# Kernel optimization log

Measured on AMD Instinct MI355X. Metric: run time of the kernel, lower is better.

## Reference

```python
import jax, jax.numpy as jnp
import numpy as np

N_PATCHES = 14
HIDDEN_D = 768
N_HEADS = 12
D_HEAD = HIDDEN_D // N_HEADS
SEQ = N_PATCHES ** 2 + 1  # 197
INPUT_D = 3 * 16 * 16  # c * patch_h * patch_w = 768
LN_EPS = 1e-5


def positional_embeddings(seq_len, d):
    # result[i, j] = sin(i / 10000**(j/d)) if j even else cos(i / 10000**((j-1)/d))
    i = jnp.arange(seq_len, dtype=jnp.float32)[:, None]
    j = jnp.arange(d, dtype=jnp.float32)[None, :]
    even = (jnp.arange(d) % 2 == 0)[None, :]
    denom_even = jnp.power(10000.0, j / d)
    denom_odd = jnp.power(10000.0, (j - 1.0) / d)
    return jnp.where(even, jnp.sin(i / denom_even), jnp.cos(i / denom_odd))


def setup_inputs() -> dict:
    key = jax.random.key(0)
    ks = jax.random.split(key, 12)
    s = 0.02
    return {
        "images": jax.random.normal(ks[0], (128, 3, 224, 224), dtype=jnp.float32),
        "W_map": jax.random.normal(ks[1], (HIDDEN_D, INPUT_D), dtype=jnp.float32) * s,
        "b_map": jax.random.normal(ks[2], (HIDDEN_D,), dtype=jnp.float32) * s,
        "class_token": jax.random.uniform(ks[3], (1, HIDDEN_D), dtype=jnp.float32),
        "ln_w": jnp.ones((SEQ, HIDDEN_D), dtype=jnp.float32),
        "ln_b": jnp.zeros((SEQ, HIDDEN_D), dtype=jnp.float32),
        "Wq": jax.random.normal(ks[4], (N_HEADS, D_HEAD, D_HEAD), dtype=jnp.float32) * s,
        "bq": jax.random.normal(ks[5], (N_HEADS, D_HEAD), dtype=jnp.float32) * s,
        "Wk": jax.random.normal(ks[6], (N_HEADS, D_HEAD, D_HEAD), dtype=jnp.float32) * s,
        "bk": jax.random.normal(ks[7], (N_HEADS, D_HEAD), dtype=jnp.float32) * s,
        "Wv": jax.random.normal(ks[8], (N_HEADS, D_HEAD, D_HEAD), dtype=jnp.float32) * s,
        "bv": jax.random.normal(ks[9], (N_HEADS, D_HEAD), dtype=jnp.float32) * s,
    }


def _forward(images, W_map, b_map, class_token, ln_w, ln_b, Wq, bq, Wk, bk, Wv, bv):
    n = images.shape[0]
    # naive patchify (faithful to source: a plain reshape)
    patches = images.reshape(n, N_PATCHES ** 2, INPUT_D)
    # linear mapper: x @ W.T + b
    tokens = jnp.einsum("npi,di->npd", patches, W_map) + b_map
    # prepend class token
    cls = jnp.broadcast_to(class_token[None], (n, 1, HIDDEN_D))
    tokens = jnp.concatenate([cls, tokens], axis=1)  # [n, SEQ, D]
    # positional embeddings
    tokens = tokens + positional_embeddings(SEQ, HIDDEN_D)[None]
    # LayerNorm over last two dims (SEQ, D) jointly
    mean = jnp.mean(tokens, axis=(-2, -1), keepdims=True)
    var = jnp.var(tokens, axis=(-2, -1), keepdims=True)
    x = (tokens - mean) / jnp.sqrt(var + LN_EPS) * ln_w + ln_b
    # multi-head self-attention (batched over samples and heads)
    xh = x.reshape(n, SEQ, N_HEADS, D_HEAD)  # head-sliced channels
    q = jnp.einsum("bshd,hed->bshe", xh, Wq) + bq[None, None]
    k = jnp.einsum("bshd,hed->bshe", xh, Wk) + bk[None, None]
    v = jnp.einsum("bshd,hed->bshe", xh, Wv) + bv[None, None]
    att = jax.nn.softmax(
        jnp.einsum("bshd,bthd->bhst", q, k) / jnp.sqrt(jnp.float32(D_HEAD)), axis=-1
    )
    msa = jnp.einsum("bhst,bthd->bshd", att, v).reshape(n, SEQ, HIDDEN_D)
    return tokens + msa


def reference(images, W_map, b_map, class_token, ln_w, ln_b, Wq, bq, Wk, bk, Wv, bv):
    return _forward(images, W_map, b_map, class_token, ln_w, ln_b, Wq, bq, Wk, bk, Wv, bv)
```

## Files before the change

### kernel.cpp

```cpp
#include <hip/hip_runtime.h>

typedef float fx4 __attribute__((ext_vector_type(4)));
typedef __bf16 bf16x8 __attribute__((ext_vector_type(8)));
typedef unsigned short ushort8 __attribute__((ext_vector_type(8)));
typedef unsigned int uint2v __attribute__((ext_vector_type(2)));
typedef unsigned int uint4v __attribute__((ext_vector_type(4)));

#define MFMA16(a, b, c) __builtin_amdgcn_mfma_f32_16x16x32_bf16((a), (b), (c), 0, 0, 0)

#if __has_builtin(__builtin_amdgcn_exp2f)
#define EXP2(x) __builtin_amdgcn_exp2f(x)
#else
#define EXP2(x) exp2f(x)
#endif

__device__ __forceinline__ unsigned short f2bf(float f) {
  return __builtin_bit_cast(unsigned short, (__bf16)f);
}

__device__ __forceinline__ ushort8 pack8(fx4 a, fx4 b) {
  ushort8 v;
  v[0] = f2bf(a[0]); v[1] = f2bf(a[1]); v[2] = f2bf(a[2]); v[3] = f2bf(a[3]);
  v[4] = f2bf(b[0]); v[5] = f2bf(b[1]); v[6] = f2bf(b[2]); v[7] = f2bf(b[3]);
  return v;
}

__device__ __forceinline__ uint2v pack2(fx4 v) {
  uint2v r;
  r[0] = (unsigned int)f2bf(v[0]) | ((unsigned int)f2bf(v[1]) << 16);
  r[1] = (unsigned int)f2bf(v[2]) | ((unsigned int)f2bf(v[3]) << 16);
  return r;
}

__device__ __forceinline__ uint2v preswap(uint2v x, int presrc) {
  uint2v r;
  r[0] = (unsigned int)__shfl((int)x[0], presrc, 64);
  r[1] = (unsigned int)__shfl((int)x[1], presrc, 64);
  return r;
}

__device__ __forceinline__ bf16x8 xfrm2(uint2v As, uint2v Bs) {
  unsigned int a0 = As[0], b0 = Bs[0], a1 = As[1], b1 = Bs[1];
  asm("v_permlane32_swap_b32 %0, %1" : "+v"(a0), "+v"(b0));
  asm("v_permlane32_swap_b32 %0, %1" : "+v"(a1), "+v"(b1));
  uint4v pf;
  pf[0] = a0; pf[1] = a1; pf[2] = b0; pf[3] = b1;
  return __builtin_bit_cast(bf16x8, pf);
}

__device__ __forceinline__ void gl2lds16(const unsigned short* g, void* lds_base) {
  __builtin_amdgcn_global_load_lds(
      (const __attribute__((address_space(1))) void*)(unsigned long long)(g),
      (__attribute__((address_space(3))) void*)(unsigned int)(unsigned long long)(lds_base),
      16, 0, 0);
}

__global__ void k_pe(float* __restrict__ pe, float* __restrict__ sums, float* __restrict__ sqs) {
  int idx = blockIdx.x * 256 + threadIdx.x;
  int s = idx / 768;
  int j = idx - s * 768;
  int jj = j & ~1;
  float ang = (float)s * expf((float)jj * (-9.210340371976184f / 768.0f));
  pe[idx] = (j & 1) ? cosf(ang) : sinf(ang);
  if (blockIdx.x == 0 && threadIdx.x < 128) {
    sums[threadIdx.x] = 0.f;
    sqs[threadIdx.x] = 0.f;
  }
}

__global__ void k_cvt(const float* __restrict__ img, const float* __restrict__ W,
                      unsigned short* __restrict__ imgbf, unsigned short* __restrict__ wbf) {
  size_t i = ((size_t)blockIdx.x * 256 + threadIdx.x) * 8;
  const float* src;
  unsigned short* dst;
  if (i < 19267584) { src = img + i; dst = imgbf + i; }
  else { size_t j = i - 19267584; src = W + j; dst = wbf + j; }
  const fx4* p = (const fx4*)src;
  *(ushort8*)dst = pack8(p[0], p[1]);
}

__global__ void k_wcvt(const float* __restrict__ Wq, const float* __restrict__ Wk,
                       const float* __restrict__ Wv, unsigned short* __restrict__ wqkv) {
  int i = (blockIdx.x * 256 + threadIdx.x) * 8;
  const float* src = (i < 49152) ? (Wq + i) : (i < 98304 ? Wk + (i - 49152) : Wv + (i - 98304));
  const fx4* p = (const fx4*)src;
  *(ushort8*)(wqkv + i) = pack8(p[0], p[1]);
}

__global__ __launch_bounds__(256) void k_tokens(
    const unsigned short* __restrict__ imgbf, const unsigned short* __restrict__ wbf,
    const float* __restrict__ bmap, const float* __restrict__ pe,
    float* __restrict__ out, float* __restrict__ sums, float* __restrict__ sqs) {
  __shared__ __align__(16) ushort8 Sf[16 * 64];
  if (blockIdx.x >= 196) return;
  const int tid = threadIdx.x;
  const int m0 = blockIdx.x * 128;
  const int n0 = blockIdx.y * 128;
  const int lane = tid & 63;
  const int w = tid >> 6;
  const int quad = lane >> 4, l16 = lane & 15;
  const int m_off = (w & 1) * 64, n_off = (w >> 1) * 64;

  fx4 acc[4][4];
#pragma unroll
  for (int i = 0; i < 4; i++)
#pragma unroll
    for (int j = 0; j < 4; j++) acc[i][j] = (fx4){0.f, 0.f, 0.f, 0.f};

  const unsigned short* pA = imgbf + (size_t)(m0 + w * 16 + l16) * 768 + quad * 8;
  const unsigned short* pB = wbf + (size_t)(n0 + w * 16 + l16) * 768 + quad * 8;
  void* lA0 = (void*)&Sf[(w) * 64];
  void* lA1 = (void*)&Sf[(4 + w) * 64];
  void* lB0 = (void*)&Sf[(8 + w) * 64];
  void* lB1 = (void*)&Sf[(12 + w) * 64];

  for (int k0 = 0; k0 < 768; k0 += 32) {
    __syncthreads();
    gl2lds16(pA + k0, lA0);
    gl2lds16(pA + 64 * 768 + k0, lA1);
    gl2lds16(pB + k0, lB0);
    gl2lds16(pB + 64 * 768 + k0, lB1);
    __syncthreads();
    bf16x8 a[4], b[4];
#pragma unroll
    for (int mt = 0; mt < 4; mt++)
      a[mt] = __builtin_bit_cast(bf16x8, Sf[((w & 1) * 4 + mt) * 64 + lane]);
#pragma unroll
    for (int nt = 0; nt < 4; nt++)
      b[nt] = __builtin_bit_cast(bf16x8, Sf[(8 + (w >> 1) * 4 + nt) * 64 + lane]);
#pragma unroll
    for (int mt = 0; mt < 4; mt++)
#pragma unroll
      for (int nt = 0; nt < 4; nt++) acc[mt][nt] = MFMA16(a[mt], b[nt], acc[mt][nt]);
  }

  float s0 = 0.f, q0 = 0.f, s1 = 0.f, q1 = 0.f;
  const int b0 = m0 / 196;
#pragma unroll
  for (int mt = 0; mt < 4; mt++) {
#pragma unroll
    for (int nt = 0; nt < 4; nt++) {
      const int col = n0 + n_off + nt * 16 + l16;
      const float bc = bmap[col];
#pragma unroll
      for (int r = 0; r < 4; r++) {
        const int gm = m0 + m_off + mt * 16 + quad * 4 + r;
        const int bb = gm / 196;
        const int ss = gm - bb * 196 + 1;
        float val = acc[mt][nt][r] + bc + pe[ss * 768 + col];
        out[((size_t)bb * 197 + ss) * 768 + col] = val;
        if (bb == b0) { s0 += val; q0 += val * val; }
        else          { s1 += val; q1 += val * val; }
      }
    }
  }
  for (int off = 32; off > 0; off >>= 1) {
    s0 += __shfl_down(s0, off); q0 += __shfl_down(q0, off);
    s1 += __shfl_down(s1, off); q1 += __shfl_down(q1, off);
  }
  if (lane == 0) {
    atomicAdd(&sums[b0], s0);
    atomicAdd(&sqs[b0], q0);
    if (b0 + 1 < 128) { atomicAdd(&sums[b0 + 1], s1); atomicAdd(&sqs[b0 + 1], q1); }
  }
}

__global__ __launch_bounds__(256) void k_cls(
    const float* __restrict__ ct, const float* __restrict__ pe,
    float* __restrict__ out, float* __restrict__ sums, float* __restrict__ sqs) {
  const int b = blockIdx.x, tid = threadIdx.x;
  float s = 0.f, q = 0.f;
#pragma unroll
  for (int it = 0; it < 3; it++) {
    int j = tid + it * 256;
    float v = ct[j] + pe[j];
    out[(size_t)b * 197 * 768 + j] = v;
    s += v; q += v * v;
  }
  for (int off = 32; off > 0; off >>= 1) { s += __shfl_down(s, off); q += __shfl_down(q, off); }
  __shared__ float rs[4], rq[4];
  int w = tid >> 6;
  if ((tid & 63) == 0) { rs[w] = s; rq[w] = q; }
  __syncthreads();
  if (tid == 0) {
    atomicAdd(&sums[b], rs[0] + rs[1] + rs[2] + rs[3]);
    atomicAdd(&sqs[b], rq[0] + rq[1] + rq[2] + rq[3]);
  }
}

__global__ void k_fin(const float* __restrict__ sums, const float* __restrict__ sqs,
                      float* __restrict__ mr) {
  int i = threadIdx.x;
  const float inv = 1.0f / 151296.0f;
  float m = sums[i] * inv;
  float v = sqs[i] * inv - m * m;
  mr[2 * i] = m;
  mr[2 * i + 1] = rsqrtf(v + 1e-5f);
}

__global__ __launch_bounds__(512, 4) void k_fused(
    const float* tok, const float* __restrict__ mr,
    const float* __restrict__ lnw, const float* __restrict__ lnb,
    const unsigned short* __restrict__ wqkv,
    const float* __restrict__ bq, const float* __restrict__ bk, const float* __restrict__ bv,
    float* out) {
  __shared__ __align__(16) ushort8 Kf[26 * 64];
  __shared__ __align__(16) ushort8 Vf[24 * 64];
  __shared__ __align__(16) ushort8 Vt[4 * 32];
  const int tid = threadIdx.x;
  const int bh = blockIdx.x;
  const int b = bh / 12;
  const int h = bh - b * 12;
  const int lane = tid & 63;
  const int w = tid >> 6;
  const int quad = lane >> 4;
  const int l16 = lane & 15;
  const int presrc = ((quad + 1) & 2) ? (lane ^ 48) : lane;
  const float mean = mr[2 * b], rstd = mr[2 * b + 1];
  const int hcol = h * 64;

  bf16x8 qfr[2][2];

  if (w < 7) {
    const int jp = w;
    bf16x8 wq[4][2], wk[4][2], wv[4][2];
#pragma unroll
    for (int et = 0; et < 4; et++) {
      const int ro = (et * 16 + l16) * 64 + quad * 8;
#pragma unroll
      for (int kk = 0; kk < 2; kk++) {
        wq[et][kk] = *(const bf16x8*)(wqkv + hcol * 64 + ro + kk * 32);
        wk[et][kk] = *(const bf16x8*)(wqkv + 49152 + hcol * 64 + ro + kk * 32);
        wv[et][kk] = *(const bf16x8*)(wqkv + 98304 + hcol * 64 + ro + kk * 32);
      }
    }
    bf16x8 xf[2][2];
#pragma unroll
    for (int s2 = 0; s2 < 2; s2++) {
      const int tt = 2 * jp + s2;
      if (tt < 13) {
        int ss = tt * 16 + l16;
        ss = (ss < 197) ? ss : 196;
#pragma unroll
        for (int kk = 0; kk < 2; kk++) {
          const int col = hcol + kk * 32 + quad * 8;
          const fx4* px = (const fx4*)(tok + (size_t)(b * 197 + ss) * 768 + col);
          const fx4* pw = (const fx4*)(lnw + (size_t)ss * 768 + col);
          const fx4* pb = (const fx4*)(lnb + (size_t)ss * 768 + col);
          fx4 y0 = (px[0] - mean) * rstd * pw[0] + pb[0];
          fx4 y1 = (px[1] - mean) * rstd * pw[1] + pb[1];
          xf[s2][kk] = __builtin_bit_cast(bf16x8, pack8(y0, y1));
        }
        fx4 aq[4], ak[4];
#pragma unroll
        for (int et = 0; et < 4; et++) {
          aq[et] = (fx4){0.f, 0.f, 0.f, 0.f};
          ak[et] = (fx4){0.f, 0.f, 0.f, 0.f};
        }
#pragma unroll
        for (int kk = 0; kk < 2; kk++)
#pragma unroll
          for (int et = 0; et < 4; et++) {
            aq[et] = MFMA16(wq[et][kk], xf[s2][kk], aq[et]);
            ak[et] = MFMA16(wk[et][kk], xf[s2][kk], ak[et]);
          }
        uint2v qp[4], kp[4];
#pragma unroll
        for (int et = 0; et < 4; et++) {
          fx4 bqv = *(const fx4*)(bq + hcol + et * 16 + quad * 4);
          fx4 bkv = *(const fx4*)(bk + hcol + et * 16 + quad * 4);
          qp[et] = preswap(pack2((aq[et] + bqv) * 0.18033688f), presrc);
          kp[et] = preswap(pack2(ak[et] + bkv), presrc);
        }
#pragma unroll
        for (int kk = 0; kk < 2; kk++) {
          qfr[s2][kk] = xfrm2(qp[2 * kk], qp[2 * kk + 1]);
          bf16x8 kfrag = xfrm2(kp[2 * kk], kp[2 * kk + 1]);
          Kf[(tt * 2 + kk) * 64 + lane] = __builtin_bit_cast(ushort8, kfrag);
        }
      }
    }
    fx4 av[2][4];
#pragma unroll
    for (int s2 = 0; s2 < 2; s2++)
#pragma unroll
      for (int et = 0; et < 4; et++) av[s2][et] = (fx4){0.f, 0.f, 0.f, 0.f};
#pragma unroll
    for (int s2 = 0; s2 < 2; s2++) {
      const int tt = 2 * jp + s2;
      if (tt < 13) {
#pragma unroll
        for (int kk = 0; kk < 2; kk++)
#pragma unroll
          for (int et = 0; et < 4; et++)
            av[s2][et] = MFMA16(xf[s2][kk], wv[et][kk], av[s2][et]);
      }
    }
#pragma unroll
    for (int et = 0; et < 4; et++) {
      const float bvv = bv[hcol + et * 16 + l16];
      fx4 bb4 = (fx4){bvv, bvv, bvv, bvv};
      uint2v v0 = preswap(pack2(av[0][et] + bb4), presrc);
      uint2v v1 = preswap(pack2(av[1][et] + bb4), presrc);
      bf16x8 vfrag = xfrm2(v0, v1);
      if (jp < 6) Vf[(et * 6 + jp) * 64 + lane] = __builtin_bit_cast(ushort8, vfrag);
      else if (quad < 2) Vt[et * 32 + lane] = __builtin_bit_cast(ushort8, vfrag);
    }
  }
  __syncthreads();

#pragma unroll
  for (int qi = 0; qi < 2; qi++) {
    const int mt = 2 * w + qi;
    if (mt < 13) {
      const int sg = mt * 16 + l16;
      const int sgc = (sg < 197) ? sg : 196;
      float* op = out + ((size_t)b * 197 + sgc) * 768 + hcol + quad * 4;
      fx4 ocur[4];
#pragma unroll
      for (int et = 0; et < 4; et++) ocur[et] = *(const fx4*)(op + et * 16);

      fx4 sacc[13];
#pragma unroll
      for (int nt = 0; nt < 13; nt++) sacc[nt] = (fx4){0.f, 0.f, 0.f, 0.f};
#pragma unroll
      for (int kk = 0; kk < 2; kk++) {
        bf16x8 qf = qfr[qi][kk];
#pragma unroll
        for (int nt = 0; nt < 13; nt++) {
          bf16x8 kf = __builtin_bit_cast(bf16x8, Kf[(nt * 2 + kk) * 64 + lane]);
          sacc[nt] = MFMA16(kf, qf, sacc[nt]);
        }
      }
      float sm = 0.f;
      uint2v pk[13];
#pragma unroll
      for (int nt = 0; nt < 13; nt++) {
        fx4 p;
#pragma unroll
        for (int r = 0; r < 4; r++) {
          const bool valid = (nt < 12) | (quad * 4 + r < 5);
          p[r] = valid ? EXP2(sacc[nt][r]) : 0.f;
          sm += p[r];
        }
        pk[nt] = preswap(pack2(p), presrc);
      }
      sm += __shfl_xor(sm, 16);
      sm += __shfl_xor(sm, 32);
      const float inv = 1.0f / sm;

      fx4 oacc[4];
#pragma unroll
      for (int et = 0; et < 4; et++) oacc[et] = (fx4){0.f, 0.f, 0.f, 0.f};
#pragma unroll
      for (int kk = 0; kk < 7; kk++) {
        bf16x8 pfrag;
        if (kk < 6) {
          pfrag = xfrm2(pk[2 * kk], pk[2 * kk + 1]);
        } else {
          uint2v z2; z2[0] = 0u; z2[1] = 0u;
          pfrag = xfrm2(pk[12], z2);
        }
#pragma unroll
        for (int et = 0; et < 4; et++) {
          bf16x8 vf;
          if (kk < 6) {
            vf = __builtin_bit_cast(bf16x8, Vf[(et * 6 + kk) * 64 + lane]);
          } else if (quad < 2) {
            vf = __builtin_bit_cast(bf16x8, Vt[et * 32 + lane]);
          } else {
            ushort8 z = {0, 0, 0, 0, 0, 0, 0, 0};
            vf = __builtin_bit_cast(bf16x8, z);
          }
          oacc[et] = MFMA16(vf, pfrag, oacc[et]);
        }
      }
      if (sg < 197) {
#pragma unroll
        for (int et = 0; et < 4; et++) {
          *(fx4*)(op + et * 16) = ocur[et] + oacc[et] * inv;
        }
      }
    }
  }
}

extern "C" void kernel_launch(void* const* d_in, const int* in_sizes, int n_in,
                              void* d_out, int out_size, void* d_ws, size_t ws_size,
                              hipStream_t stream) {
  (void)in_sizes; (void)n_in; (void)out_size; (void)ws_size;
  const float* img  = (const float*)d_in[0];
  const float* Wmap = (const float*)d_in[1];
  const float* bmap = (const float*)d_in[2];
  const float* ct   = (const float*)d_in[3];
  const float* lnw  = (const float*)d_in[4];
  const float* lnb  = (const float*)d_in[5];
  const float* Wq   = (const float*)d_in[6];
  const float* bq   = (const float*)d_in[7];
  const float* Wk   = (const float*)d_in[8];
  const float* bk   = (const float*)d_in[9];
  const float* Wv   = (const float*)d_in[10];
  const float* bv   = (const float*)d_in[11];
  float* out = (float*)d_out;

  float* pe   = (float*)d_ws;
  float* sums = pe + 151296;
  float* sqs  = sums + 128;
  float* mr   = sqs + 128;
  unsigned short* wbf   = (unsigned short*)(mr + 256);
  unsigned short* imgbf = wbf + 589824;
  unsigned short* wqkv  = imgbf + (size_t)19267584;

  k_pe<<<591, 256, 0, stream>>>(pe, sums, sqs);
  k_cvt<<<9696, 256, 0, stream>>>(img, Wmap, imgbf, wbf);
  k_wcvt<<<72, 256, 0, stream>>>(Wq, Wk, Wv, wqkv);
  k_tokens<<<dim3(200, 6), 256, 0, stream>>>(imgbf, wbf, bmap, pe, out, sums, sqs);
  k_cls<<<128, 256, 0, stream>>>(ct, pe, out, sums, sqs);
  k_fin<<<1, 128, 0, stream>>>(sums, sqs, mr);
  k_fused<<<1536, 512, 0, stream>>>(out, mr, lnw, lnb, wqkv, bq, bk, bv, out);
}
```

Before: 371.8 us.

## Merge prep kernels, remap GEMM tiles, fold LN stats, halve attention block size

Combines positional-embedding generation, the bf16 conversions and the class-token row into one prep launch. The class-token row computes its sums directly and initialises the per-sample accumulators, which removes the separate zeroing and the atomics on that path. The token GEMM uses a 1D grid whose remapped tile order keeps neighbouring blocks on the same tiles, and the finalize kernel is dropped by computing mean and rstd inline in the attention kernel. The attention kernel now runs with 256 threads, each wave handling two projection slabs and up to four query tiles, and it reads the residual late instead of holding it in registers. This cuts launch overhead and register pressure, at the cost of more serial work per wave.

Result: faster. 353.6 us (-4.9%).

```diff
diff --git a/kernel.cpp b/kernel.cpp
--- a/kernel.cpp
+++ b/kernel.cpp
@@ -55,36 +55,54 @@
       16, 0, 0);
 }
 
-__global__ void k_pe(float* __restrict__ pe, float* __restrict__ sums, float* __restrict__ sqs) {
-  int idx = blockIdx.x * 256 + threadIdx.x;
-  int s = idx / 768;
-  int j = idx - s * 768;
-  int jj = j & ~1;
-  float ang = (float)s * expf((float)jj * (-9.210340371976184f / 768.0f));
-  pe[idx] = (j & 1) ? cosf(ang) : sinf(ang);
-  if (blockIdx.x == 0 && threadIdx.x < 128) {
-    sums[threadIdx.x] = 0.f;
-    sqs[threadIdx.x] = 0.f;
-  }
-}
-
-__global__ void k_cvt(const float* __restrict__ img, const float* __restrict__ W,
-                      unsigned short* __restrict__ imgbf, unsigned short* __restrict__ wbf) {
-  size_t i = ((size_t)blockIdx.x * 256 + threadIdx.x) * 8;
-  const float* src;
-  unsigned short* dst;
-  if (i < 19267584) { src = img + i; dst = imgbf + i; }
-  else { size_t j = i - 19267584; src = W + j; dst = wbf + j; }
-  const fx4* p = (const fx4*)src;
-  *(ushort8*)dst = pack8(p[0], p[1]);
-}
-
-__global__ void k_wcvt(const float* __restrict__ Wq, const float* __restrict__ Wk,
-                       const float* __restrict__ Wv, unsigned short* __restrict__ wqkv) {
-  int i = (blockIdx.x * 256 + threadIdx.x) * 8;
-  const float* src = (i < 49152) ? (Wq + i) : (i < 98304 ? Wk + (i - 49152) : Wv + (i - 98304));
-  const fx4* p = (const fx4*)src;
-  *(ushort8*)(wqkv + i) = pack8(p[0], p[1]);
+__global__ __launch_bounds__(256) void k_prep(
+    const float* __restrict__ img, const float* __restrict__ W,
+    const float* __restrict__ Wq, const float* __restrict__ Wk, const float* __restrict__ Wv,
+    const float* __restrict__ ct,
+    float* __restrict__ pe, unsigned short* __restrict__ imgbf, unsigned short* __restrict__ wbf,
+    unsigned short* __restrict__ wqkv,
+    float* __restrict__ out, float* __restrict__ sums, float* __restrict__ sqs) {
+  const int bid = blockIdx.x, tid = threadIdx.x;
+  if (bid < 591) {
+    int idx = bid * 256 + tid;
+    int s = idx / 768;
+    int j = idx - s * 768;
+    int jj = j & ~1;
+    float ang = (float)s * expf((float)jj * (-9.210340371976184f / 768.0f));
+    pe[idx] = (j & 1) ? cosf(ang) : sinf(ang);
+  } else if (bid < 10287) {
+    size_t i = ((size_t)(bid - 591) * 256 + tid) * 8;
+    const float* src;
+    unsigned short* dst;
+    if (i < 19267584) { src = img + i; dst = imgbf + i; }
+    else { size_t j = i - 19267584; src = W + j; dst = wbf + j; }
+    const fx4* p = (const fx4*)src;
+    *(ushort8*)dst = pack8(p[0], p[1]);
+  } else if (bid < 10359) {
+    int i = ((bid - 10287) * 256 + tid) * 8;
+    const float* src = (i < 49152) ? (Wq + i) : (i < 98304 ? Wk + (i - 49152) : Wv + (i - 98304));
+    const fx4* p = (const fx4*)src;
+    *(ushort8*)(wqkv + i) = pack8(p[0], p[1]);
+  } else {
+    const int b = bid - 10359;
+    float s = 0.f, q = 0.f;
+#pragma unroll
+    for (int it = 0; it < 3; it++) {
+      int j = tid + it * 256;
+      float v = ct[j] + ((j & 1) ? 1.f : 0.f);
+      out[(size_t)b * 197 * 768 + j] = v;
+      s += v; q += v * v;
+    }
+    for (int off = 32; off > 0; off >>= 1) { s += __shfl_down(s, off); q += __shfl_down(q, off); }
+    __shared__ float rs[4], rq[4];
+    int w = tid >> 6;
+    if ((tid & 63) == 0) { rs[w] = s; rq[w] = q; }
+    __syncthreads();
+    if (tid == 0) {
+      sums[b] = rs[0] + rs[1] + rs[2] + rs[3];
+      sqs[b] = rq[0] + rq[1] + rq[2] + rq[3];
+    }
+  }
 }
 
 __global__ __launch_bounds__(256) void k_tokens(
@@ -92,10 +110,10 @@
     const float* __restrict__ bmap, const float* __restrict__ pe,
     float* __restrict__ out, float* __restrict__ sums, float* __restrict__ sqs) {
   __shared__ __align__(16) ushort8 Sf[16 * 64];
-  if (blockIdx.x >= 196) return;
   const int tid = threadIdx.x;
-  const int m0 = blockIdx.x * 128;
-  const int n0 = blockIdx.y * 128;
+  const int idx = (blockIdx.x & 7) * 147 + (blockIdx.x >> 3);
+  const int m0 = (idx / 6) * 128;
+  const int n0 = (idx % 6) * 128;
   const int lane = tid & 63;
   const int w = tid >> 6;
   const int quad = lane >> 4, l16 = lane & 15;
@@ -165,41 +183,8 @@
   }
 }
 
-__global__ __launch_bounds__(256) void k_cls(
-    const float* __restrict__ ct, const float* __restrict__ pe,
-    float* __restrict__ out, float* __restrict__ sums, float* __restrict__ sqs) {
-  const int b = blockIdx.x, tid = threadIdx.x;
-  float s = 0.f, q = 0.f;
-#pragma unroll
-  for (int it = 0; it < 3; it++) {
-    int j = tid + it * 256;
-    float v = ct[j] + pe[j];
-    out[(size_t)b * 197 * 768 + j] = v;
-    s += v; q += v * v;
-  }
-  for (int off = 32; off > 0; off >>= 1) { s += __shfl_down(s, off); q += __shfl_down(q, off); }
-  __shared__ float rs[4], rq[4];
-  int w = tid >> 6;
-  if ((tid & 63) == 0) { rs[w] = s; rq[w] = q; }
-  __syncthreads();
-  if (tid == 0) {
-    atomicAdd(&sums[b], rs[0] + rs[1] + rs[2] + rs[3]);
-    atomicAdd(&sqs[b], rq[0] + rq[1] + rq[2] + rq[3]);
-  }
-}
-
-__global__ void k_fin(const float* __restrict__ sums, const float* __restrict__ sqs,
-                      float* __restrict__ mr) {
-  int i = threadIdx.x;
-  const float inv = 1.0f / 151296.0f;
-  float m = sums[i] * inv;
-  float v = sqs[i] * inv - m * m;
-  mr[2 * i] = m;
-  mr[2 * i + 1] = rsqrtf(v + 1e-5f);
-}
-
-__global__ __launch_bounds__(512, 4) void k_fused(
-    const float* tok, const float* __restrict__ mr,
+__global__ __launch_bounds__(256, 3) void k_fused(
+    const float* tok, const float* __restrict__ sums, const float* __restrict__ sqs,
     const float* __restrict__ lnw, const float* __restrict__ lnb,
     const unsigned short* __restrict__ wqkv,
     const float* __restrict__ bq, const float* __restrict__ bk, const float* __restrict__ bv,
@@ -216,110 +201,110 @@
   const int quad = lane >> 4;
   const int l16 = lane & 15;
   const int presrc = ((quad + 1) & 2) ? (lane ^ 48) : lane;
-  const float mean = mr[2 * b], rstd = mr[2 * b + 1];
+  const float invN = 1.0f / 151296.0f;
+  const float mean = sums[b] * invN;
+  const float rstd = rsqrtf(sqs[b] * invN - mean * mean + 1e-5f);
   const int hcol = h * 64;
 
-  bf16x8 qfr[2][2];
-
-  if (w < 7) {
-    const int jp = w;
-    bf16x8 wq[4][2], wk[4][2], wv[4][2];
-#pragma unroll
-    for (int et = 0; et < 4; et++) {
-      const int ro = (et * 16 + l16) * 64 + quad * 8;
-#pragma unroll
-      for (int kk = 0; kk < 2; kk++) {
-        wq[et][kk] = *(const bf16x8*)(wqkv + hcol * 64 + ro + kk * 32);
-        wk[et][kk] = *(const bf16x8*)(wqkv + 49152 + hcol * 64 + ro + kk * 32);
-        wv[et][kk] = *(const bf16x8*)(wqkv + 98304 + hcol * 64 + ro + kk * 32);
-      }
-    }
-    bf16x8 xf[2][2];
-#pragma unroll
-    for (int s2 = 0; s2 < 2; s2++) {
-      const int tt = 2 * jp + s2;
-      if (tt < 13) {
-        int ss = tt * 16 + l16;
-        ss = (ss < 197) ? ss : 196;
-#pragma unroll
-        for (int kk = 0; kk < 2; kk++) {
-          const int col = hcol + kk * 32 + quad * 8;
-          const fx4* px = (const fx4*)(tok + (size_t)(b * 197 + ss) * 768 + col);
-          const fx4* pw = (const fx4*)(lnw + (size_t)ss * 768 + col);
-          const fx4* pb = (const fx4*)(lnb + (size_t)ss * 768 + col);
-          fx4 y0 = (px[0] - mean) * rstd * pw[0] + pb[0];
-          fx4 y1 = (px[1] - mean) * rstd * pw[1] + pb[1];
-          xf[s2][kk] = __builtin_bit_cast(bf16x8, pack8(y0, y1));
-        }
-        fx4 aq[4], ak[4];
-#pragma unroll
-        for (int et = 0; et < 4; et++) {
-          aq[et] = (fx4){0.f, 0.f, 0.f, 0.f};
-          ak[et] = (fx4){0.f, 0.f, 0.f, 0.f};
-        }
-#pragma unroll
-        for (int kk = 0; kk < 2; kk++)
+  bf16x8 qfr[4][2];
+
+  bf16x8 wq[4][2], wk[4][2], wv[4][2];
+#pragma unroll
+  for (int et = 0; et < 4; et++) {
+    const int ro = (et * 16 + l16) * 64 + quad * 8;
+#pragma unroll
+    for (int kk = 0; kk < 2; kk++) {
+      wq[et][kk] = *(const bf16x8*)(wqkv + hcol * 64 + ro + kk * 32);
+      wk[et][kk] = *(const bf16x8*)(wqkv + 49152 + hcol * 64 + ro + kk * 32);
+      wv[et][kk] = *(const bf16x8*)(wqkv + 98304 + hcol * 64 + ro + kk * 32);
+    }
+  }
+
+#pragma unroll
+  for (int pi = 0; pi < 2; pi++) {
+    const int jp = w + 4 * pi;
+    if (jp <= 6) {
+      bf16x8 xf[2][2];
+#pragma unroll
+      for (int s2 = 0; s2 < 2; s2++) {
+        const int tt = 2 * jp + s2;
+        if (tt < 13) {
+          int ss = tt * 16 + l16;
+          ss = (ss < 197) ? ss : 196;
+#pragma unroll
+          for (int kk = 0; kk < 2; kk++) {
+            const int col = hcol + kk * 32 + quad * 8;
+            const fx4* px = (const fx4*)(tok + (size_t)(b * 197 + ss) * 768 + col);
+            const fx4* pw = (const fx4*)(lnw + (size_t)ss * 768 + col);
+            const fx4* pb = (const fx4*)(lnb + (size_t)ss * 768 + col);
+            fx4 y0 = (px[0] - mean) * rstd * pw[0] + pb[0];
+            fx4 y1 = (px[1] - mean) * rstd * pw[1] + pb[1];
+            xf[s2][kk] = __builtin_bit_cast(bf16x8, pack8(y0, y1));
+          }
+          fx4 aq[4], ak[4];
 #pragma unroll
           for (int et = 0; et < 4; et++) {
-            aq[et] = MFMA16(wq[et][kk], xf[s2][kk], aq[et]);
-            ak[et] = MFMA16(wk[et][kk], xf[s2][kk], ak[et]);
+            aq[et] = (fx4){0.f, 0.f, 0.f, 0.f};
+            ak[et] = (fx4){0.f, 0.f, 0.f, 0.f};
           }
-        uint2v qp[4], kp[4];
-#pragma unroll
-        for (int et = 0; et < 4; et++) {
-          fx4 bqv = *(const fx4*)(bq + hcol + et * 16 + quad * 4);
-          fx4 bkv = *(const fx4*)(bk + hcol + et * 16 + quad * 4);
-          qp[et] = preswap(pack2((aq[et] + bqv) * 0.18033688f), presrc);
-          kp[et] = preswap(pack2(ak[et] + bkv), presrc);
-        }
-#pragma unroll
-        for (int kk = 0; kk < 2; kk++) {
-          qfr[s2][kk] = xfrm2(qp[2 * kk], qp[2 * kk + 1]);
-          bf16x8 kfrag = xfrm2(kp[2 * kk], kp[2 * kk + 1]);
-          Kf[(tt * 2 + kk) * 64 + lane] = __builtin_bit_cast(ushort8, kfrag);
-        }
-      }
-    }
-    fx4 av[2][4];
-#pragma unroll
-    for (int s2 = 0; s2 < 2; s2++)
-#pragma unroll
-      for (int et = 0; et < 4; et++) av[s2][et] = (fx4){0.f, 0.f, 0.f, 0.f};
-#pragma unroll
-    for (int s2 = 0; s2 < 2; s2++) {
-      const int tt = 2 * jp + s2;
-      if (tt < 13) {
-#pragma unroll
-        for (int kk = 0; kk < 2; kk++)
-#pragma unroll
-          for (int et = 0; et < 4; et++)
-            av[s2][et] = MFMA16(xf[s2][kk], wv[et][kk], av[s2][et]);
-      }
-    }
-#pragma unroll
-    for (int et = 0; et < 4; et++) {
-      const float bvv = bv[hcol + et * 16 + l16];
-      fx4 bb4 = (fx4){bvv, bvv, bvv, bvv};
-      uint2v v0 = preswap(pack2(av[0][et] + bb4), presrc);
-      uint2v v1 = preswap(pack2(av[1][et] + bb4), presrc);
-      bf16x8 vfrag = xfrm2(v0, v1);
-      if (jp < 6) Vf[(et * 6 + jp) * 64 + lane] = __builtin_bit_cast(ushort8, vfrag);
-      else if (quad < 2) Vt[et * 32 + lane] = __builtin_bit_cast(ushort8, vfrag);
+#pragma unroll
+          for (int kk = 0; kk < 2; kk++)
+#pragma unroll
+            for (int et = 0; et < 4; et++) {
+              aq[et] = MFMA16(wq[et][kk], xf[s2][kk], aq[et]);
+              ak[et] = MFMA16(wk[et][kk], xf[s2][kk], ak[et]);
+            }
+          uint2v qp[4], kp[4];
+#pragma unroll
+          for (int et = 0; et < 4; et++) {
+            fx4 bqv = *(const fx4*)(bq + hcol + et * 16 + quad * 4);
+            fx4 bkv = *(const fx4*)(bk + hcol + et * 16 + quad * 4);
+            qp[et] = preswap(pack2((aq[et] + bqv) * 0.18033688f), presrc);
+            kp[et] = preswap(pack2(ak[et] + bkv), presrc);
+          }
+          const int qi = pi * 2 + s2;
+#pragma unroll
+          for (int kk = 0; kk < 2; kk++) {
+            qfr[qi][kk] = xfrm2(qp[2 * kk], qp[2 * kk + 1]);
+            bf16x8 kfrag = xfrm2(kp[2 * kk], kp[2 * kk + 1]);
+            Kf[(tt * 2 + kk) * 64 + lane] = __builtin_bit_cast(ushort8, kfrag);
+          }
+        }
+      }
+      fx4 av[2][4];
+#pragma unroll
+      for (int s2 = 0; s2 < 2; s2++)
+#pragma unroll
+        for (int et = 0; et < 4; et++) av[s2][et] = (fx4){0.f, 0.f, 0.f, 0.f};
+#pragma unroll
+      for (int s2 = 0; s2 < 2; s2++) {
+        const int tt = 2 * jp + s2;
+        if (tt < 13) {
+#pragma unroll
+          for (int kk = 0; kk < 2; kk++)
+#pragma unroll
+            for (int et = 0; et < 4; et++)
+              av[s2][et] = MFMA16(xf[s2][kk], wv[et][kk], av[s2][et]);
+        }
+      }
+#pragma unroll
+      for (int et = 0; et < 4; et++) {
+        const float bvv = bv[hcol + et * 16 + l16];
+        fx4 bb4 = (fx4){bvv, bvv, bvv, bvv};
+        uint2v v0 = preswap(pack2(av[0][et] + bb4), presrc);
+        uint2v v1 = preswap(pack2(av[1][et] + bb4), presrc);
+        bf16x8 vfrag = xfrm2(v0, v1);
+        if (jp < 6) Vf[(et * 6 + jp) * 64 + lane] = __builtin_bit_cast(ushort8, vfrag);
+        else if (quad < 2) Vt[et * 32 + lane] = __builtin_bit_cast(ushort8, vfrag);
+      }
     }
   }
   __syncthreads();
 
 #pragma unroll
-  for (int qi = 0; qi < 2; qi++) {
-    const int mt = 2 * w + qi;
+  for (int qi = 0; qi < 4; qi++) {
+    const int mt = 2 * w + (qi >> 1) * 8 + (qi & 1);
     if (mt < 13) {
-      const int sg = mt * 16 + l16;
-      const int sgc = (sg < 197) ? sg : 196;
-      float* op = out + ((size_t)b * 197 + sgc) * 768 + hcol + quad * 4;
-      fx4 ocur[4];
-#pragma unroll
-      for (int et = 0; et < 4; et++) ocur[et] = *(const fx4*)(op + et * 16);
-
       fx4 sacc[13];
 #pragma unroll
       for (int nt = 0; nt < 13; nt++) sacc[nt] = (fx4){0.f, 0.f, 0.f, 0.f};
@@ -375,10 +360,14 @@
           oacc[et] = MFMA16(vf, pfrag, oacc[et]);
         }
       }
+      const int sg = mt * 16 + l16;
       if (sg < 197) {
+        float* op = out + ((size_t)b * 197 + sg) * 768 + hcol + quad * 4;
 #pragma unroll
         for (int et = 0; et < 4; et++) {
-          *(fx4*)(op + et * 16) = ocur[et] + oacc[et] * inv;
+          fx4 cur = *(const fx4*)(op + et * 16);
+          cur += oacc[et] * inv;
+          *(fx4*)(op + et * 16) = cur;
         }
       }
     }
@@ -406,16 +395,12 @@
   float* pe   = (float*)d_ws;
   float* sums = pe + 151296;
   float* sqs  = sums + 128;
-  float* mr   = sqs + 128;
-  unsigned short* wbf   = (unsigned short*)(mr + 256);
+  unsigned short* wbf   = (unsigned short*)(sqs + 128);
   unsigned short* imgbf = wbf + 589824;
   unsigned short* wqkv  = imgbf + (size_t)19267584;
 
-  k_pe<<<591, 256, 0, stream>>>(pe, sums, sqs);
-  k_cvt<<<9696, 256, 0, stream>>>(img, Wmap, imgbf, wbf);
-  k_wcvt<<<72, 256, 0, stream>>>(Wq, Wk, Wv, wqkv);
-  k_tokens<<<dim3(200, 6), 256, 0, stream>>>(imgbf, wbf, bmap, pe, out, sums, sqs);
-  k_cls<<<128, 256, 0, stream>>>(ct, pe, out, sums, sqs);
-  k_fin<<<1, 128, 0, stream>>>(sums, sqs, mr);
-  k_fused<<<1536, 512, 0, stream>>>(out, mr, lnw, lnb, wqkv, bq, bk, bv, out);
-}
+  k_prep<<<10487, 256, 0, stream>>>(img, Wmap, Wq, Wk, Wv, ct,
+                                    pe, imgbf, wbf, wqkv, out, sums, sqs);
+  k_tokens<<<1176, 256, 0, stream>>>(imgbf, wbf, bmap, pe, out, sums, sqs);
+  k_fused<<<1536, 256, 0, stream>>>(out, sums, sqs, lnw, lnb, wqkv, bq, bk, bv, out);
+}
```
